# Optimization experiments

Measured on AMD Instinct MI355X. Metric: run time of the kernel, lower is better.

The kernel has to match this reference:

```python
import jax, jax.numpy as jnp
import numpy as np

D = 64          # d_in
NH = [256, 256] # nn_depth_design
L = 16          # flow_layers
B = 32768       # batch of samples


def _build_masks():
    # Deterministic mask maps: this_min=0, this_max=d_in-1 for all layers
    mh0 = np.arange(NH[0]) % (D - 1)
    mh1 = np.arange(NH[1]) % (D - 1)
    M1 = (mh0[None, :] <= mh1[:, None]).astype(np.float32)  # [nh1, nh0]
    M0s, M2s = [], []
    for l in range(L):
        perm = np.arange(D) if l % 2 == 0 else np.arange(D)[::-1]
        M0s.append((perm[None, :] <= mh0[:, None]).astype(np.float32))  # [nh0, D]
        M2s.append((mh1[None, :] < perm[:, None]).astype(np.float32))  # [D, nh1]
    M0 = np.stack(M0s)                                   # [L, nh0, D]
    M1 = np.broadcast_to(M1, (L,) + M1.shape).copy()     # [L, nh1, nh0]
    M2 = np.stack(M2s)                                   # [L, D, nh1]
    return jnp.asarray(M0), jnp.asarray(M1), jnp.asarray(M2)


def setup_inputs() -> dict:
    key = jax.random.key(0)
    ks = jax.random.split(key, 13)
    u = jax.random.normal(ks[0], (B, D), dtype=jnp.float32)

    def w(k, shape, fan_in):
        return jax.random.uniform(k, shape, jnp.float32, -1.0, 1.0) / np.sqrt(fan_in)

    inp = {"u": u}
    i = 1
    for net in ("loc", "scale"):
        inp[f"{net}_W0"] = w(ks[i], (L, NH[0], D), D); i += 1
        inp[f"{net}_b0"] = w(ks[i], (L, NH[0]), D); i += 1
        inp[f"{net}_W1"] = w(ks[i], (L, NH[1], NH[0]), NH[0]); i += 1
        inp[f"{net}_b1"] = w(ks[i], (L, NH[1]), NH[0]); i += 1
        inp[f"{net}_W2"] = w(ks[i], (L, D, NH[1]), NH[1]); i += 1
        inp[f"{net}_b2"] = w(ks[i], (L, D), NH[1]); i += 1
    M0, M1, M2 = _build_masks()
    inp["M0"], inp["M1"], inp["M2"] = M0, M1, M2
    return inp


def reference(u, loc_W0, loc_b0, loc_W1, loc_b1, loc_W2, loc_b2,
              scale_W0, scale_b0, scale_W1, scale_b1, scale_W2, scale_b2,
              M0, M1, M2):
    def step(y, p):
        (lW0, lb0, lW1, lb1, lW2, lb2,
         sW0, sb0, sW1, sb1, sW2, sb2, m0, m1, m2) = p

        def net(W0, b0, W1, b1, W2, b2):
            h = jax.nn.relu(y @ (m0 * W0).T + b0)    # [B, nh0]
            h = jax.nn.relu(h @ (m1 * W1).T + b1)    # [B, nh1]
            return h @ (m2 * W2).T + b2              # [B, D]

        loc = net(lW0, lb0, lW1, lb1, lW2, lb2)
        sc = net(sW0, sb0, sW1, sb1, sW2, sb2)
        # inverse=False coupling: exp(-scale) * (y - loc)
        return jnp.exp(-sc) * (y - loc), None

    params = (loc_W0, loc_b0, loc_W1, loc_b1, loc_W2, loc_b2,
              scale_W0, scale_b0, scale_W1, scale_b1, scale_W2, scale_b2,
              M0, M1, M2)
    y, _ = jax.lax.scan(step, u, params)
    return y
```

## Files before the change

### kernel.cpp

```cpp
#include <hip/hip_runtime.h>
#include <hip/hip_bf16.h>

typedef __bf16 bf16x8 __attribute__((ext_vector_type(8)));
typedef __bf16 bf16x4 __attribute__((ext_vector_type(4)));
typedef float  f32x4  __attribute__((ext_vector_type(4)));

#define LAYERS 16
#define DIM 64
#define NHID 256
#define BATCH 32768
#define MTILE 64
#define NBLOCKS (BATCH / MTILE)

#define W0P_PER 16384
#define W1P_PER 65536
#define W2P_PER 16384
#define W0P_TOT (32 * W0P_PER)
#define W1P_TOT (32 * W1P_PER)
#define W2P_TOT (32 * W2P_PER)
#define PACK_TOT (W0P_TOT + W1P_TOT + W2P_TOT)

__device__ __forceinline__ bf16x8 ldw(const __bf16* p) { return *(const bf16x8*)p; }

__global__ __launch_bounds__(256) void pack_weights(
    const float* __restrict__ lW0, const float* __restrict__ lW1, const float* __restrict__ lW2,
    const float* __restrict__ sW0, const float* __restrict__ sW1, const float* __restrict__ sW2,
    __bf16* __restrict__ ws)
{
    const long i = ((long)blockIdx.x * 256 + threadIdx.x) * 8;
    const float* W; long src; int l, n, k, which;
    if (i < W0P_TOT) {
        int netl = (int)(i / W0P_PER), rem = (int)(i % W0P_PER);
        int net = netl >> 4; l = netl & 15;
        int nt = rem >> 10, kt = (rem >> 9) & 1, lane = (rem >> 3) & 63;
        n = nt * 16 + (lane & 15); k = kt * 32 + (lane >> 4) * 8;
        W = net ? sW0 : lW0; which = 0;
        src = (long)(l * 256 + n) * 64 + k;
    } else if (i < W0P_TOT + W1P_TOT) {
        long r = i - W0P_TOT;
        int netl = (int)(r / W1P_PER), rem = (int)(r % W1P_PER);
        int net = netl >> 4; l = netl & 15;
        int nt = rem >> 12, kt = (rem >> 9) & 7, lane = (rem >> 3) & 63;
        n = nt * 16 + (lane & 15); k = kt * 32 + (lane >> 4) * 8;
        W = net ? sW1 : lW1; which = 1;
        src = (long)(l * 256 + n) * 256 + k;
    } else {
        long r = i - W0P_TOT - W1P_TOT;
        int netl = (int)(r / W2P_PER), rem = (int)(r % W2P_PER);
        int net = netl >> 4; l = netl & 15;
        int nt = rem >> 12, kt = (rem >> 9) & 7, lane = (rem >> 3) & 63;
        n = nt * 16 + (lane & 15); k = kt * 32 + (lane >> 4) * 8;
        W = net ? sW2 : lW2; which = 2;
        src = (long)(l * 64 + n) * 256 + k;
    }
    f32x4 wa = *(const f32x4*)(W + src);
    f32x4 wb = *(const f32x4*)(W + src + 4);
    const int nm = n % 63;
    const int pn = (l & 1) ? 63 - n : n;
    bf16x8 o;
    #pragma unroll
    for (int j = 0; j < 8; ++j) {
        int kk = k + j;
        bool m;
        if (which == 0)      { int pk = (l & 1) ? 63 - kk : kk; m = (pk <= nm); }
        else if (which == 1) { m = ((kk % 63) <= nm); }
        else                 { m = ((kk % 63) < pn); }
        float v = (j < 4) ? wa[j] : wb[j - 4];
        o[j] = m ? (__bf16)v : (__bf16)0.0f;
    }
    *(bf16x8*)(ws + i) = o;
}

__global__ void __launch_bounds__(256, 2)
flow_kernel(
    const float* __restrict__ u,
    const __bf16* __restrict__ wp,
    const float* __restrict__ lb0, const float* __restrict__ lb1, const float* __restrict__ lb2,
    const float* __restrict__ sb0, const float* __restrict__ sb1, const float* __restrict__ sb2,
    float* __restrict__ out)
{
    __shared__ __bf16 ybf[4 * 2 * 512];
    __shared__ __bf16 buf1[4 * 8 * 512];
    __shared__ __bf16 buf2[4 * 8 * 512];

    const int tid  = threadIdx.x;
    const int wave = tid >> 6;
    const int lane = tid & 63;
    const int quad = lane >> 4;
    const int l16  = lane & 15;
    const int blk  = blockIdx.x;

    const int qh = quad >> 1;
    const int qp = (quad & 1) * 4;

    const __bf16* w0p = wp;
    const __bf16* w1p = wp + W0P_TOT;
    const __bf16* w2p = wp + W0P_TOT + W1P_TOT;

    f32x4 y[4];
    #pragma unroll
    for (int bt = 0; bt < 4; ++bt)
        y[bt] = *(const f32x4*)(u + (long)(blk * MTILE + bt * 16 + l16) * DIM
                                  + wave * 16 + quad * 4);

    const int ktY = wave >> 1;
    const int flY = ((wave & 1) * 2 + qh) * 16 + l16;

    bf16x8 wg1[8];
    #pragma unroll
    for (int ot = 0; ot < 4; ++ot)
        #pragma unroll
        for (int kt = 0; kt < 2; ++kt)
            wg1[ot * 2 + kt] = ldw(w0p + (long)((4 * wave + ot) * 2 + kt) * 512 + lane * 8);

    for (int l = 0; l < LAYERS; ++l) {
        #pragma unroll
        for (int bt = 0; bt < 4; ++bt) {
            bf16x4 v;
            #pragma unroll
            for (int r = 0; r < 4; ++r) v[r] = (__bf16)y[bt][r];
            *(bf16x4*)&ybf[((bt * 2 + ktY) * 64 + flY) * 8 + qp] = v;
        }
        __syncthreads();

        f32x4 locr[4], scr[4];

        #pragma unroll
        for (int net = 0; net < 2; ++net) {
            const __bf16* w1b = w1p + (long)(net * 16 + l) * W1P_PER;
            const __bf16* w2b = w2p + (long)(net * 16 + l) * W2P_PER;
            const __bf16* w0n = w0p + (long)(net == 0 ? 16 + l : l + 1) * W0P_PER;
            const float* b0 = (net ? sb0 : lb0) + l * 256;
            const float* b1 = (net ? sb1 : lb1) + l * 256;
            const float* b2 = (net ? sb2 : lb2) + l * 64;

            bf16x8 wg2a[16];

            {
                f32x4 acc[4][4];
                #pragma unroll
                for (int ot = 0; ot < 4; ++ot)
                    #pragma unroll
                    for (int bt = 0; bt < 4; ++bt)
                        acc[ot][bt] = (f32x4){0.f, 0.f, 0.f, 0.f};
                #pragma unroll
                for (int kt = 0; kt < 2; ++kt) {
                    bf16x8 bv[4];
                    #pragma unroll
                    for (int bt = 0; bt < 4; ++bt)
                        bv[bt] = *(const bf16x8*)&ybf[((bt * 2 + kt) * 64 + lane) * 8];
                    #pragma unroll
                    for (int ot = 0; ot < 4; ++ot)
                        #pragma unroll
                        for (int bt = 0; bt < 4; ++bt)
                            acc[ot][bt] = __builtin_amdgcn_mfma_f32_16x16x32_bf16(wg1[ot * 2 + kt], bv[bt], acc[ot][bt], 0, 0, 0);
                }
                #pragma unroll
                for (int kt = 0; kt < 4; ++kt)
                    #pragma unroll
                    for (int ot = 0; ot < 4; ++ot)
                        wg2a[kt * 4 + ot] = ldw(w1b + (long)((4 * wave + ot) * 8 + kt) * 512 + lane * 8);
                #pragma unroll
                for (int ot = 0; ot < 4; ++ot) {
                    f32x4 bias = *(const f32x4*)(b0 + (4 * wave + ot) * 16 + quad * 4);
                    const int kt1 = (4 * wave + ot) >> 1;
                    const int fl  = ((ot & 1) * 2 + qh) * 16 + l16;
                    #pragma unroll
                    for (int bt = 0; bt < 4; ++bt) {
                        bf16x4 v;
                        #pragma unroll
                        for (int r = 0; r < 4; ++r)
                            v[r] = (__bf16)fmaxf(acc[ot][bt][r] + bias[r], 0.f);
                        *(bf16x4*)&buf1[((bt * 8 + kt1) * 64 + fl) * 8 + qp] = v;
                    }
                }
            }
            __syncthreads();

            bf16x8 wg3[8];

            {
                f32x4 acc[4][4];
                #pragma unroll
                for (int ot = 0; ot < 4; ++ot)
                    #pragma unroll
                    for (int bt = 0; bt < 4; ++bt)
                        acc[ot][bt] = (f32x4){0.f, 0.f, 0.f, 0.f};
                #pragma unroll
                for (int kt = 0; kt < 8; ++kt) {
                    bf16x8 aw[4];
                    #pragma unroll
                    for (int ot = 0; ot < 4; ++ot)
                        aw[ot] = (kt < 4) ? wg2a[kt * 4 + ot]
                                          : ldw(w1b + (long)((4 * wave + ot) * 8 + kt) * 512 + lane * 8);
                    bf16x8 bv[4];
                    #pragma unroll
                    for (int bt = 0; bt < 4; ++bt)
                        bv[bt] = *(const bf16x8*)&buf1[((bt * 8 + kt) * 64 + lane) * 8];
                    #pragma unroll
                    for (int ot = 0; ot < 4; ++ot)
                        #pragma unroll
                        for (int bt = 0; bt < 4; ++bt)
                            acc[ot][bt] = __builtin_amdgcn_mfma_f32_16x16x32_bf16(aw[ot], bv[bt], acc[ot][bt], 0, 0, 0);
                }
                #pragma unroll
                for (int ot = 0; ot < 4; ++ot) {
                    f32x4 bias = *(const f32x4*)(b1 + (4 * wave + ot) * 16 + quad * 4);
                    const int kt1 = (4 * wave + ot) >> 1;
                    const int fl  = ((ot & 1) * 2 + qh) * 16 + l16;
                    #pragma unroll
                    for (int bt = 0; bt < 4; ++bt) {
                        bf16x4 v;
                        #pragma unroll
                        for (int r = 0; r < 4; ++r)
                            v[r] = (__bf16)fmaxf(acc[ot][bt][r] + bias[r], 0.f);
                        *(bf16x4*)&buf2[((bt * 8 + kt1) * 64 + fl) * 8 + qp] = v;
                    }
                }
                #pragma unroll
                for (int kt = 0; kt < 8; ++kt)
                    wg3[kt] = ldw(w2b + (long)(wave * 8 + kt) * 512 + lane * 8);
            }
            __syncthreads();

            {
                f32x4 acc[4];
                #pragma unroll
                for (int bt = 0; bt < 4; ++bt)
                    acc[bt] = (f32x4){0.f, 0.f, 0.f, 0.f};
                #pragma unroll
                for (int kt = 0; kt < 8; ++kt) {
                    #pragma unroll
                    for (int bt = 0; bt < 4; ++bt) {
                        bf16x8 bv = *(const bf16x8*)&buf2[((bt * 8 + kt) * 64 + lane) * 8];
                        acc[bt] = __builtin_amdgcn_mfma_f32_16x16x32_bf16(wg3[kt], bv, acc[bt], 0, 0, 0);
                    }
                }
                #pragma unroll
                for (int ot = 0; ot < 4; ++ot)
                    #pragma unroll
                    for (int kt = 0; kt < 2; ++kt)
                        wg1[ot * 2 + kt] = ldw(w0n + (long)((4 * wave + ot) * 2 + kt) * 512 + lane * 8);
                f32x4 bias = *(const f32x4*)(b2 + wave * 16 + quad * 4);
                if (net == 0) {
                    #pragma unroll
                    for (int bt = 0; bt < 4; ++bt)
                        #pragma unroll
                        for (int r = 0; r < 4; ++r)
                            locr[bt][r] = acc[bt][r] + bias[r];
                } else {
                    #pragma unroll
                    for (int bt = 0; bt < 4; ++bt)
                        #pragma unroll
                        for (int r = 0; r < 4; ++r)
                            scr[bt][r] = acc[bt][r] + bias[r];
                }
            }
        }

        #pragma unroll
        for (int bt = 0; bt < 4; ++bt)
            #pragma unroll
            for (int r = 0; r < 4; ++r)
                y[bt][r] = __expf(-scr[bt][r]) * (y[bt][r] - locr[bt][r]);
    }

    #pragma unroll
    for (int bt = 0; bt < 4; ++bt)
        *(f32x4*)(out + (long)(blk * MTILE + bt * 16 + l16) * DIM
                      + wave * 16 + quad * 4) = y[bt];
}

extern "C" void kernel_launch(void* const* d_in, const int* in_sizes, int n_in,
                              void* d_out, int out_size, void* d_ws, size_t ws_size,
                              hipStream_t stream) {
    const float* u   = (const float*)d_in[0];
    const float* lW0 = (const float*)d_in[1];
    const float* lb0 = (const float*)d_in[2];
    const float* lW1 = (const float*)d_in[3];
    const float* lb1 = (const float*)d_in[4];
    const float* lW2 = (const float*)d_in[5];
    const float* lb2 = (const float*)d_in[6];
    const float* sW0 = (const float*)d_in[7];
    const float* sb0 = (const float*)d_in[8];
    const float* sW1 = (const float*)d_in[9];
    const float* sb1 = (const float*)d_in[10];
    const float* sW2 = (const float*)d_in[11];
    const float* sb2 = (const float*)d_in[12];

    if (ws_size < (size_t)PACK_TOT * sizeof(__bf16)) return;
    __bf16* ws = (__bf16*)d_ws;

    pack_weights<<<PACK_TOT / 8 / 256, 256, 0, stream>>>(
        lW0, lW1, lW2, sW0, sW1, sW2, ws);
    flow_kernel<<<NBLOCKS, 256, 0, stream>>>(
        u, ws, lb0, lb1, lb2, sb0, sb1, sb2, (float*)d_out);
}
```

Before: 315.9 us.

## Split each 64-row tile across 8 waves instead of 4

The flow kernel now launches 512 threads per block. The output-feature work of each hidden layer is split across 8 waves, each handling 2 output tiles instead of 4. The final 64-wide layer is split by output tile and batch half. This roughly halves per-wave register use (accumulators and weight fragments) so more waves can be resident and latency hiding improves. The cost is that each weight fragment is loaded by more waves per tile, and block-wide barriers now synchronize more waves.

```diff
diff --git a/kernel.cpp b/kernel.cpp
--- a/kernel.cpp
+++ b/kernel.cpp
@@ -71,7 +71,7 @@
     *(bf16x8*)(ws + i) = o;
 }
 
-__global__ void __launch_bounds__(256, 2)
+__global__ void __launch_bounds__(512, 4)
 flow_kernel(
     const float* __restrict__ u,
     const __bf16* __restrict__ wp,
@@ -84,7 +84,7 @@
     __shared__ __bf16 buf2[4 * 8 * 512];
 
     const int tid  = threadIdx.x;
-    const int wave = tid >> 6;
+    const int w    = tid >> 6;
     const int lane = tid & 63;
     const int quad = lane >> 4;
     const int l16  = lane & 15;
@@ -93,37 +93,40 @@
     const int qh = quad >> 1;
     const int qp = (quad & 1) * 4;
 
+    const int otD = w >> 1;
+    const int bh  = w & 1;
+
     const __bf16* w0p = wp;
     const __bf16* w1p = wp + W0P_TOT;
     const __bf16* w2p = wp + W0P_TOT + W1P_TOT;
 
-    f32x4 y[4];
-    #pragma unroll
-    for (int bt = 0; bt < 4; ++bt)
-        y[bt] = *(const f32x4*)(u + (long)(blk * MTILE + bt * 16 + l16) * DIM
-                                  + wave * 16 + quad * 4);
-
-    const int ktY = wave >> 1;
-    const int flY = ((wave & 1) * 2 + qh) * 16 + l16;
-
-    bf16x8 wg1[8];
-    #pragma unroll
-    for (int ot = 0; ot < 4; ++ot)
+    f32x4 y[2];
+    #pragma unroll
+    for (int bt = 0; bt < 2; ++bt)
+        y[bt] = *(const f32x4*)(u + (long)(blk * MTILE + bh * 32 + bt * 16 + l16) * DIM
+                                  + otD * 16 + quad * 4);
+
+    const int ktY = w >> 2;
+    const int flY = ((((w >> 1) & 1) * 2 + qh) * 16 + l16);
+
+    bf16x8 wg1[4];
+    #pragma unroll
+    for (int oi = 0; oi < 2; ++oi)
         #pragma unroll
         for (int kt = 0; kt < 2; ++kt)
-            wg1[ot * 2 + kt] = ldw(w0p + (long)((4 * wave + ot) * 2 + kt) * 512 + lane * 8);
+            wg1[oi * 2 + kt] = ldw(w0p + (long)((2 * w + oi) * 2 + kt) * 512 + lane * 8);
 
     for (int l = 0; l < LAYERS; ++l) {
         #pragma unroll
-        for (int bt = 0; bt < 4; ++bt) {
+        for (int bt = 0; bt < 2; ++bt) {
             bf16x4 v;
             #pragma unroll
             for (int r = 0; r < 4; ++r) v[r] = (__bf16)y[bt][r];
-            *(bf16x4*)&ybf[((bt * 2 + ktY) * 64 + flY) * 8 + qp] = v;
+            *(bf16x4*)&ybf[(((bh * 2 + bt) * 2 + ktY) * 64 + flY) * 8 + qp] = v;
         }
         __syncthreads();
 
-        f32x4 locr[4], scr[4];
+        f32x4 locr[2], scr[2];
 
         #pragma unroll
         for (int net = 0; net < 2; ++net) {
@@ -134,15 +137,15 @@
             const float* b1 = (net ? sb1 : lb1) + l * 256;
             const float* b2 = (net ? sb2 : lb2) + l * 64;
 
-            bf16x8 wg2a[16];
+            bf16x8 wg2a[8];
 
             {
-                f32x4 acc[4][4];
-                #pragma unroll
-                for (int ot = 0; ot < 4; ++ot)
-                    #pragma unroll
-                    for (int bt = 0; bt < 4; ++bt)
-                        acc[ot][bt] = (f32x4){0.f, 0.f, 0.f, 0.f};
+                f32x4 acc[2][4];
+                #pragma unroll
+                for (int oi = 0; oi < 2; ++oi)
+                    #pragma unroll
+                    for (int bt = 0; bt < 4; ++bt)
+                        acc[oi][bt] = (f32x4){0.f, 0.f, 0.f, 0.f};
                 #pragma unroll
                 for (int kt = 0; kt < 2; ++kt) {
                     bf16x8 bv[4];
@@ -150,28 +153,27 @@
                     for (int bt = 0; bt < 4; ++bt)
                         bv[bt] = *(const bf16x8*)&ybf[((bt * 2 + kt) * 64 + lane) * 8];
                     #pragma unroll
-                    for (int ot = 0; ot < 4; ++ot)
+                    for (int oi = 0; oi < 2; ++oi)
                         #pragma unroll
                         for (int bt = 0; bt < 4; ++bt)
-                            acc[ot][bt] = __builtin_amdgcn_mfma_f32_16x16x32_bf16(wg1[ot * 2 + kt], bv[bt], acc[ot][bt], 0, 0, 0);
+                            acc[oi][bt] = __builtin_amdgcn_mfma_f32_16x16x32_bf16(wg1[oi * 2 + kt], bv[bt], acc[oi][bt], 0, 0, 0);
                 }
                 #pragma unroll
                 for (int kt = 0; kt < 4; ++kt)
                     #pragma unroll
-                    for (int ot = 0; ot < 4; ++ot)
-                        wg2a[kt * 4 + ot] = ldw(w1b + (long)((4 * wave + ot) * 8 + kt) * 512 + lane * 8);
-                #pragma unroll
-                for (int ot = 0; ot < 4; ++ot) {
-                    f32x4 bias = *(const f32x4*)(b0 + (4 * wave + ot) * 16 + quad * 4);
-                    const int kt1 = (4 * wave + ot) >> 1;
-                    const int fl  = ((ot & 1) * 2 + qh) * 16 + l16;
+                    for (int oi = 0; oi < 2; ++oi)
+                        wg2a[kt * 2 + oi] = ldw(w1b + (long)((2 * w + oi) * 8 + kt) * 512 + lane * 8);
+                #pragma unroll
+                for (int oi = 0; oi < 2; ++oi) {
+                    f32x4 bias = *(const f32x4*)(b0 + (2 * w + oi) * 16 + quad * 4);
+                    const int fl = ((oi * 2 + qh) * 16 + l16);
                     #pragma unroll
                     for (int bt = 0; bt < 4; ++bt) {
                         bf16x4 v;
                         #pragma unroll
                         for (int r = 0; r < 4; ++r)
-                            v[r] = (__bf16)fmaxf(acc[ot][bt][r] + bias[r], 0.f);
-                        *(bf16x4*)&buf1[((bt * 8 + kt1) * 64 + fl) * 8 + qp] = v;
+                            v[r] = (__bf16)fmaxf(acc[oi][bt][r] + bias[r], 0.f);
+                        *(bf16x4*)&buf1[((bt * 8 + w) * 64 + fl) * 8 + qp] = v;
                     }
                 }
             }
@@ -180,95 +182,94 @@
             bf16x8 wg3[8];
 
             {
-                f32x4 acc[4][4];
-                #pragma unroll
-                for (int ot = 0; ot < 4; ++ot)
-                    #pragma unroll
-                    for (int bt = 0; bt < 4; ++bt)
-                        acc[ot][bt] = (f32x4){0.f, 0.f, 0.f, 0.f};
+                f32x4 acc[2][4];
+                #pragma unroll
+                for (int oi = 0; oi < 2; ++oi)
+                    #pragma unroll
+                    for (int bt = 0; bt < 4; ++bt)
+                        acc[oi][bt] = (f32x4){0.f, 0.f, 0.f, 0.f};
                 #pragma unroll
                 for (int kt = 0; kt < 8; ++kt) {
-                    bf16x8 aw[4];
-                    #pragma unroll
-                    for (int ot = 0; ot < 4; ++ot)
-                        aw[ot] = (kt < 4) ? wg2a[kt * 4 + ot]
-                                          : ldw(w1b + (long)((4 * wave + ot) * 8 + kt) * 512 + lane * 8);
+                    bf16x8 aw[2];
+                    #pragma unroll
+                    for (int oi = 0; oi < 2; ++oi)
+                        aw[oi] = (kt < 4) ? wg2a[kt * 2 + oi]
+                                          : ldw(w1b + (long)((2 * w + oi) * 8 + kt) * 512 + lane * 8);
                     bf16x8 bv[4];
                     #pragma unroll
                     for (int bt = 0; bt < 4; ++bt)
                         bv[bt] = *(const bf16x8*)&buf1[((bt * 8 + kt) * 64 + lane) * 8];
                     #pragma unroll
-                    for (int ot = 0; ot < 4; ++ot)
+                    for (int oi = 0; oi < 2; ++oi)
                         #pragma unroll
                         for (int bt = 0; bt < 4; ++bt)
-                            acc[ot][bt] = __builtin_amdgcn_mfma_f32_16x16x32_bf16(aw[ot], bv[bt], acc[ot][bt], 0, 0, 0);
-                }
-                #pragma unroll
-                for (int ot = 0; ot < 4; ++ot) {
-                    f32x4 bias = *(const f32x4*)(b1 + (4 * wave + ot) * 16 + quad * 4);
-                    const int kt1 = (4 * wave + ot) >> 1;
-                    const int fl  = ((ot & 1) * 2 + qh) * 16 + l16;
+                            acc[oi][bt] = __builtin_amdgcn_mfma_f32_16x16x32_bf16(aw[oi], bv[bt], acc[oi][bt], 0, 0, 0);
+                }
+                #pragma unroll
+                for (int oi = 0; oi < 2; ++oi) {
+                    f32x4 bias = *(const f32x4*)(b1 + (2 * w + oi) * 16 + quad * 4);
+                    const int fl = ((oi * 2 + qh) * 16 + l16);
                     #pragma unroll
                     for (int bt = 0; bt < 4; ++bt) {
                         bf16x4 v;
                         #pragma unroll
                         for (int r = 0; r < 4; ++r)
-                            v[r] = (__bf16)fmaxf(acc[ot][bt][r] + bias[r], 0.f);
-                        *(bf16x4*)&buf2[((bt * 8 + kt1) * 64 + fl) * 8 + qp] = v;
+                            v[r] = (__bf16)fmaxf(acc[oi][bt][r] + bias[r], 0.f);
+                        *(bf16x4*)&buf2[((bt * 8 + w) * 64 + fl) * 8 + qp] = v;
                     }
                 }
                 #pragma unroll
                 for (int kt = 0; kt < 8; ++kt)
-                    wg3[kt] = ldw(w2b + (long)(wave * 8 + kt) * 512 + lane * 8);
+                    wg3[kt] = ldw(w2b + (long)(otD * 8 + kt) * 512 + lane * 8);
             }
             __syncthreads();
 
             {
-                f32x4 acc[4];
-                #pragma unroll
-                for (int bt = 0; bt < 4; ++bt)
-                    acc[bt] = (f32x4){0.f, 0.f, 0.f, 0.f};
+                f32x4 acc3[2];
+                #pragma unroll
+                for (int bt = 0; bt < 2; ++bt)
+                    acc3[bt] = (f32x4){0.f, 0.f, 0.f, 0.f};
                 #pragma unroll
                 for (int kt = 0; kt < 8; ++kt) {
                     #pragma unroll
-                    for (int bt = 0; bt < 4; ++bt) {
-                        bf16x8 bv = *(const bf16x8*)&buf2[((bt * 8 + kt) * 64 + lane) * 8];
-                        acc[bt] = __builtin_amdgcn_mfma_f32_16x16x32_bf16(wg3[kt], bv, acc[bt], 0, 0, 0);
+                    for (int bt = 0; bt < 2; ++bt) {
+                        bf16x8 bv = *(const bf16x8*)&buf2[(((bh * 2 + bt) * 8 + kt) * 64 + lane) * 8];
+                        acc3[bt] = __builtin_amdgcn_mfma_f32_16x16x32_bf16(wg3[kt], bv, acc3[bt], 0, 0, 0);
                     }
                 }
                 #pragma unroll
-                for (int ot = 0; ot < 4; ++ot)
+                for (int oi = 0; oi < 2; ++oi)
                     #pragma unroll
                     for (int kt = 0; kt < 2; ++kt)
-                        wg1[ot * 2 + kt] = ldw(w0n + (long)((4 * wave + ot) * 2 + kt) * 512 + lane * 8);
-                f32x4 bias = *(const f32x4*)(b2 + wave * 16 + quad * 4);
+                        wg1[oi * 2 + kt] = ldw(w0n + (long)((2 * w + oi) * 2 + kt) * 512 + lane * 8);
+                f32x4 bias = *(const f32x4*)(b2 + otD * 16 + quad * 4);
                 if (net == 0) {
                     #pragma unroll
-                    for (int bt = 0; bt < 4; ++bt)
-                        #pragma unroll
-                        for (int r = 0; r < 4; ++r)
-                            locr[bt][r] = acc[bt][r] + bias[r];
+                    for (int bt = 0; bt < 2; ++bt)
+                        #pragma unroll
+                        for (int r = 0; r < 4; ++r)
+                            locr[bt][r] = acc3[bt][r] + bias[r];
                 } else {
                     #pragma unroll
-                    for (int bt = 0; bt < 4; ++bt)
-                        #pragma unroll
-                        for (int r = 0; r < 4; ++r)
-                            scr[bt][r] = acc[bt][r] + bias[r];
+                    for (int bt = 0; bt < 2; ++bt)
+                        #pragma unroll
+                        for (int r = 0; r < 4; ++r)
+                            scr[bt][r] = acc3[bt][r] + bias[r];
                 }
             }
         }
 
         #pragma unroll
-        for (int bt = 0; bt < 4; ++bt)
+        for (int bt = 0; bt < 2; ++bt)
             #pragma unroll
             for (int r = 0; r < 4; ++r)
                 y[bt][r] = __expf(-scr[bt][r]) * (y[bt][r] - locr[bt][r]);
     }
 
     #pragma unroll
-    for (int bt = 0; bt < 4; ++bt)
-        *(f32x4*)(out + (long)(blk * MTILE + bt * 16 + l16) * DIM
-                      + wave * 16 + quad * 4) = y[bt];
+    for (int bt = 0; bt < 2; ++bt)
+        *(f32x4*)(out + (long)(blk * MTILE + bh * 32 + bt * 16 + l16) * DIM
+                      + otD * 16 + quad * 4) = y[bt];
 }
 
 extern "C" void kernel_launch(void* const* d_in, const int* in_sizes, int n_in,
@@ -293,6 +294,6 @@
 
     pack_weights<<<PACK_TOT / 8 / 256, 256, 0, stream>>>(
         lW0, lW1, lW2, sW0, sW1, sW2, ws);
-    flow_kernel<<<NBLOCKS, 256, 0, stream>>>(
+    flow_kernel<<<NBLOCKS, 512, 0, stream>>>(
         u, ws, lb0, lb1, lb2, sb0, sb1, sb2, (float*)d_out);
 }
```

New measurement: 299.7 us. -5.1%, faster.
